# Kernel optimization log

Hardware: AMD Instinct MI355X
Metric: run time of the kernel (lower is better)

## Reference

```python
import jax, jax.numpy as jnp
import numpy as np

D = 1024      # embedding_dim
H = 16        # n_heads
HD = D // H   # head_dim
EPS = 1e-05


def layernorm(x, scale, bias):
    # torch.var default is unbiased (ddof=1) in the original module
    mean = jnp.mean(x, axis=-1, keepdims=True)
    var = jnp.var(x, axis=-1, keepdims=True, ddof=1)
    return scale * (x - mean) / jnp.sqrt(var + EPS) + bias


def gelu(x):
    return 0.5 * x * (1 + jnp.tanh(0.79788456 * (x + 0.044715 * x ** 3)))


def setup_inputs() -> dict:
    key = jax.random.key(0)
    ks = jax.random.split(key, 12)
    s = 0.02
    return {
        "x": jax.random.normal(ks[0], (2, 2048, D), dtype=jnp.float32),
        "Wq": jax.random.normal(ks[1], (D, D), dtype=jnp.float32) * s,
        "Wk": jax.random.normal(ks[2], (D, D), dtype=jnp.float32) * s,
        "Wv": jax.random.normal(ks[3], (D, D), dtype=jnp.float32) * s,
        "Wo": jax.random.normal(ks[4], (D, D), dtype=jnp.float32) * s,
        "bo": jnp.zeros((D,), dtype=jnp.float32),
        "W1": jax.random.normal(ks[5], (D, 4 * D), dtype=jnp.float32) * s,
        "b1": jnp.zeros((4 * D,), dtype=jnp.float32),
        "W2": jax.random.normal(ks[6], (4 * D, D), dtype=jnp.float32) * s,
        "b2": jnp.zeros((D,), dtype=jnp.float32),
        "ln1_scale": jnp.ones((D,), dtype=jnp.float32),
        "ln1_bias": jnp.zeros((D,), dtype=jnp.float32),
        "ln2_scale": jnp.ones((D,), dtype=jnp.float32),
        "ln2_bias": jnp.zeros((D,), dtype=jnp.float32),
    }


def reference(x, Wq, Wk, Wv, Wo, bo, W1, b1, W2, b2,
              ln1_scale, ln1_bias, ln2_scale, ln2_bias):
    B, S, _ = x.shape
    # --- attention sub-block (pre-LN) ---
    h = layernorm(x, ln1_scale, ln1_bias)
    q = (h @ Wq).reshape(B, S, H, HD).transpose(0, 2, 1, 3)  # [B,H,S,HD]
    k = (h @ Wk).reshape(B, S, H, HD).transpose(0, 2, 1, 3)
    v = (h @ Wv).reshape(B, S, H, HD).transpose(0, 2, 1, 3)
    scores = jnp.einsum("bhqd,bhkd->bhqk", q, k)             # [B,H,S,S]
    causal = jnp.tril(jnp.ones((S, S), dtype=bool))
    scores = jnp.where(causal, scores, -jnp.inf)
    attn = jax.nn.softmax(scores / jnp.sqrt(jnp.float32(HD)), axis=-1)
    ctx = jnp.einsum("bhqk,bhkd->bhqd", attn, v)
    ctx = ctx.transpose(0, 2, 1, 3).reshape(B, S, H * HD)
    x = x + (ctx @ Wo + bo)
    # --- FFN sub-block (pre-LN) ---
    h = layernorm(x, ln2_scale, ln2_bias)
    x = x + (gelu(h @ W1 + b1) @ W2 + b2)
    return x
```

## Files before the change

### kernel.cpp

```cpp
#include <hip/hip_runtime.h>
#include <hip/hip_bf16.h>
#include <cstdint>

#define D_DIM 1024
#define S_DIM 2048
#define B_DIM 2
#define NROWS 4096
#define H_DIM 16
#define LOG2E 1.4426950408889634f
#define QSCALE (0.125f * LOG2E)

typedef __bf16 bf16x8 __attribute__((ext_vector_type(8)));
typedef float f32x4 __attribute__((ext_vector_type(4)));
typedef unsigned short u16x8 __attribute__((ext_vector_type(8)));

#define MFMA16(a, b, c) __builtin_amdgcn_mfma_f32_16x16x32_bf16(a, b, c, 0, 0, 0)
#define SBM __builtin_amdgcn_sched_barrier(0x0F)
#define WBAR __builtin_amdgcn_s_barrier()
#define VMW(n) asm volatile("s_waitcnt vmcnt(" #n ")" ::: "memory")

__device__ __forceinline__ void async_cp16(const void* g, void* lds) {
  __builtin_amdgcn_global_load_lds(
      (const __attribute__((address_space(1))) void*)(uintptr_t)g,
      (__attribute__((address_space(3))) void*)(uint32_t)(uintptr_t)lds, 16, 0, 0);
}

__device__ __forceinline__ unsigned short f2bf(float f) {
  __hip_bfloat16 h = __float2bfloat16(f);
  return __builtin_bit_cast(unsigned short, h);
}

__device__ __forceinline__ float bf2f(unsigned short u) {
  return __builtin_bit_cast(float, (unsigned int)u << 16);
}

__device__ __forceinline__ float gelu_fast(float v) {
  float u = v * v;
  float w = v * fmaf(u, 0.044715f, 1.f);
  float e = exp2f(w * -2.3022161f);
  return v * __builtin_amdgcn_rcpf(1.f + e);
}

struct TcArgs {
  const float* src[6];
  __hip_bfloat16* dst[6];
  int K[6];
  int N[6];
  int start[6];
};

__global__ __launch_bounds__(256) void transpose_cast6_kernel(TcArgs a) {
  __shared__ float tile[32][33];
  int bid = blockIdx.x, mi = 0;
#pragma unroll
  for (int i = 1; i < 6; i++)
    if (bid >= a.start[i]) mi = i;
  const float* W = a.src[mi];
  __hip_bfloat16* Wt = a.dst[mi];
  int K = a.K[mi], N = a.N[mi];
  int rel = bid - a.start[mi];
  int tilesx = N >> 5;
  int shift = (N == 4096) ? 7 : 5;
  int n0 = (rel & (tilesx - 1)) * 32, k0 = (rel >> shift) * 32;
  int tx = threadIdx.x, ty = threadIdx.y;
#pragma unroll
  for (int i = 0; i < 32; i += 8)
    tile[ty + i][tx] = W[(size_t)(k0 + ty + i) * N + n0 + tx];
  __syncthreads();
#pragma unroll
  for (int i = 0; i < 32; i += 8)
    Wt[(size_t)(n0 + ty + i) * K + k0 + tx] = __float2bfloat16(tile[tx][ty + i]);
}

__global__ __launch_bounds__(256) void ln_kernel(
    const float* __restrict__ x, const float* __restrict__ sc,
    const float* __restrict__ bi, __hip_bfloat16* __restrict__ out) {
  int row = blockIdx.x, t = threadIdx.x;
  float4 v = ((const float4*)(x + (size_t)row * D_DIM))[t];
  float s = v.x + v.y + v.z + v.w;
  float ss = v.x * v.x + v.y * v.y + v.z * v.z + v.w * v.w;
#pragma unroll
  for (int off = 32; off > 0; off >>= 1) {
    s += __shfl_xor(s, off);
    ss += __shfl_xor(ss, off);
  }
  __shared__ float red[8];
  int wid = t >> 6;
  if ((t & 63) == 0) { red[wid] = s; red[4 + wid] = ss; }
  __syncthreads();
  s = red[0] + red[1] + red[2] + red[3];
  ss = red[4] + red[5] + red[6] + red[7];
  float mean = s * (1.f / 1024.f);
  float var = (ss - 1024.f * mean * mean) * (1.f / 1023.f);
  float inv = rsqrtf(var + 1e-5f);
  float4 scv = ((const float4*)sc)[t];
  float4 biv = ((const float4*)bi)[t];
  ushort4 o;
  o.x = f2bf(scv.x * (v.x - mean) * inv + biv.x);
  o.y = f2bf(scv.y * (v.y - mean) * inv + biv.y);
  o.z = f2bf(scv.z * (v.z - mean) * inv + biv.z);
  o.w = f2bf(scv.w * (v.w - mean) * inv + biv.w);
  ((ushort4*)(out + (size_t)row * D_DIM))[t] = o;
}

template <int EPI>
__global__ __launch_bounds__(512) void gemm256_kernel(
    const __hip_bfloat16* __restrict__ A, const __hip_bfloat16* __restrict__ Bt,
    void* __restrict__ Cout, const float* __restrict__ bias,
    __hip_bfloat16* __restrict__ qb, __hip_bfloat16* __restrict__ kb,
    unsigned short* __restrict__ vt, int strideA, int strideB) {
  __shared__ char lds[131072];
  const int t = threadIdx.x;
  const int lane = t & 63, wid = t >> 6;
  const int ql = lane & 15, g = lane >> 4;
  const int wr = wid >> 2, wc = wid & 3;
  const int m0 = blockIdx.x * 256, n0 = blockIdx.y * 256;
  const int koff = blockIdx.z * 1024;
  const int sw = (ql & 7) << 4;

  const int srow = t >> 3;
  const int scol = ((t & 7) << 4) ^ ((srow & 7) << 4);
  const __hip_bfloat16* aBase = A + (size_t)(m0 + srow) * strideA + koff + (scol >> 1);
  const __hip_bfloat16* bBase = Bt + (size_t)(n0 + srow) * strideB + koff + (scol >> 1);
  const uint32_t ldsT = (uint32_t)(t * 16);

  auto stgA = [&](int kt, int h) {
    char* dst = lds + (((kt & 1) * 2 + h) * 16384) + ldsT;
    const __hip_bfloat16* src = aBase + (size_t)(h * 128) * strideA + kt * 64;
    async_cp16(src, dst);
    async_cp16(src + (size_t)64 * strideA, dst + 8192);
  };
  auto stgB = [&](int kt, int h) {
    char* dst = lds + 65536 + (((kt & 1) * 2 + h) * 16384) + ldsT;
    const __hip_bfloat16* src = bBase + (size_t)(h * 128) * strideB + kt * 64;
    async_cp16(src, dst);
    async_cp16(src + (size_t)64 * strideB, dst + 8192);
  };

  bf16x8 aR[4][2], bR[2][2][2];
  f32x4 acc[2][4][2][2] = {};

  auto ldA = [&](int slot, int mh) {
    const char* base = lds + ((slot * 2 + mh) * 16384) + (wr * 64 + ql) * 128;
#pragma unroll
    for (int mi = 0; mi < 4; mi++)
#pragma unroll
      for (int kk = 0; kk < 2; kk++)
        aR[mi][kk] = *(const bf16x8*)(base + mi * 2048 + ((kk * 64 + g * 16) ^ sw));
  };
  auto ldB = [&](int slot, int nh) {
    const char* base = lds + 65536 + ((slot * 2 + nh) * 16384) + (wc * 32 + ql) * 128;
#pragma unroll
    for (int ni = 0; ni < 2; ni++)
#pragma unroll
      for (int kk = 0; kk < 2; kk++)
        bR[nh][ni][kk] = *(const bf16x8*)(base + ni * 2048 + ((kk * 64 + g * 16) ^ sw));
  };
  auto mma = [&](int mh, int nh) {
    __builtin_amdgcn_s_setprio(1);
#pragma unroll
    for (int mi = 0; mi < 4; mi++)
#pragma unroll
      for (int ni = 0; ni < 2; ni++) {
        f32x4 c = acc[mh][mi][nh][ni];
        c = MFMA16(aR[mi][0], bR[nh][ni][0], c);
        c = MFMA16(aR[mi][1], bR[nh][ni][1], c);
        acc[mh][mi][nh][ni] = c;
      }
    __builtin_amdgcn_s_setprio(0);
  };

  stgB(0, 0); stgA(0, 0); stgB(0, 1); stgA(0, 1); stgB(1, 0);
  VMW(6); SBM; WBAR;

#pragma unroll 1
  for (int i = 0; i < 7; i++) {
    const int o = 2 * i + 1, e2 = 2 * i + 2, o2 = 2 * i + 3;
    ldA(0, 0); ldB(0, 0); stgA(o, 0);  VMW(6); SBM; WBAR; mma(0, 0);
    ldB(0, 1);            stgB(o, 1);  VMW(6); SBM; WBAR; mma(0, 1);
    ldA(0, 1);            stgA(o, 1);          SBM; WBAR; mma(1, 1);
                          stgB(e2, 0); VMW(6); SBM; WBAR; mma(1, 0);
    ldA(1, 0); ldB(1, 0); stgA(e2, 0); VMW(6); SBM; WBAR; mma(0, 0);
    ldB(1, 1);            stgB(e2, 1); VMW(6); SBM; WBAR; mma(0, 1);
    ldA(1, 1);            stgA(e2, 1);         SBM; WBAR; mma(1, 1);
                          stgB(o2, 0); VMW(6); SBM; WBAR; mma(1, 0);
  }
  ldA(0, 0); ldB(0, 0); stgA(15, 0); VMW(6); SBM; WBAR; mma(0, 0);
  ldB(0, 1);            stgB(15, 1); VMW(6); SBM; WBAR; mma(0, 1);
  ldA(0, 1);            stgA(15, 1);         SBM; WBAR; mma(1, 1);
                                     VMW(4); SBM; WBAR; mma(1, 0);
  ldA(1, 0); ldB(1, 0);              VMW(2); SBM; WBAR; mma(0, 0);
  ldB(1, 1);                         VMW(0); SBM; WBAR; mma(0, 1);
  ldA(1, 1);                                 SBM; WBAR; mma(1, 1);
                                                        mma(1, 0);

#pragma unroll
  for (int mh = 0; mh < 2; mh++) {
#pragma unroll
    for (int mi = 0; mi < 4; mi++) {
      const int row0 = m0 + mh * 128 + wr * 64 + mi * 16 + g * 4;
#pragma unroll
      for (int nh = 0; nh < 2; nh++) {
#pragma unroll
        for (int ni = 0; ni < 2; ni++) {
          const int colt = nh * 128 + wc * 32 + ni * 16 + ql;
          const f32x4 c = acc[mh][mi][nh][ni];
          if (EPI == 0) {
            const int seg = n0 >> 10;
            const int c1k = (n0 & 1023) + colt;
            if (seg < 2) {
              __hip_bfloat16* Ob = seg == 0 ? qb : kb;
              const float sc = seg == 0 ? QSCALE : 1.f;
#pragma unroll
              for (int rr = 0; rr < 4; rr++)
                Ob[(size_t)(row0 + rr) * 1024 + c1k] = __float2bfloat16(c[rr] * sc);
            } else {
              const int h = c1k >> 6, dh = c1k & 63;
              const int bb = row0 >> 11, s0 = row0 & 2047;
              ushort4 pk;
              pk.x = f2bf(c[0]); pk.y = f2bf(c[1]); pk.z = f2bf(c[2]); pk.w = f2bf(c[3]);
              *(ushort4*)(vt + (((size_t)(bb * 16 + h) * 64 + dh) << 11) + s0) = pk;
            }
          } else if (EPI == 1) {
            const int col = n0 + colt;
            const float bv = bias[col];
#pragma unroll
            for (int rr = 0; rr < 4; rr++)
              ((__hip_bfloat16*)Cout)[(size_t)(row0 + rr) * 4096 + col] =
                  __float2bfloat16(gelu_fast(c[rr] + bv));
          } else {
            unsigned short* Cp = (unsigned short*)Cout + (size_t)blockIdx.z * NROWS * 1024;
            const int col = n0 + colt;
#pragma unroll
            for (int rr = 0; rr < 4; rr++)
              Cp[(size_t)(row0 + rr) * 1024 + col] = f2bf(c[rr]);
          }
        }
      }
    }
  }
}

template <int BN, int EPI>
__global__ __launch_bounds__(256) void gemm_bt_kernel(
    const __hip_bfloat16* __restrict__ A, const __hip_bfloat16* __restrict__ Bt,
    void* __restrict__ Cout, const float* __restrict__ bias,
    const float* __restrict__ resid, int M, int N, int K, int kchunk) {
  constexpr int NBF = BN / 32;
  __shared__ __hip_bfloat16 As[2][128 * 32];
  __shared__ __hip_bfloat16 Bs[2][BN * 32];
  const int t = threadIdx.x;
  const int lane = t & 63, wid = t >> 6;
  const int ql = lane & 15, g = lane >> 4;
  const int m0 = blockIdx.x * 128, n0 = blockIdx.y * BN;
  const int kz = blockIdx.z;
  const int wm = (wid >> 1) * 64, wn = (wid & 1) * (BN / 2);
  f32x4 acc[4][NBF] = {};
  const int sr = t >> 2, sc8 = (t & 3) * 8;
  const __hip_bfloat16* ag = A + (size_t)(m0 + sr) * K + sc8 + (size_t)kz * kchunk;
  const __hip_bfloat16* bg = Bt + (size_t)(n0 + sr) * K + sc8 + (size_t)kz * kchunk;

  auto stage = [&](int buf, int k0) {
    async_cp16(ag + k0, (char*)&As[buf][0] + wid * 1024);
    async_cp16(ag + (size_t)64 * K + k0, (char*)&As[buf][0] + 4096 + wid * 1024);
    async_cp16(bg + k0, (char*)&Bs[buf][0] + wid * 1024);
    if constexpr (BN == 128)
      async_cp16(bg + (size_t)64 * K + k0, (char*)&Bs[buf][0] + 4096 + wid * 1024);
  };
  auto compute = [&](int buf) {
    bf16x8 af[4], bfr[NBF];
#pragma unroll
    for (int mb = 0; mb < 4; mb++)
      af[mb] = *(const bf16x8*)(&As[buf][(wm + mb * 16 + ql) * 32 + g * 8]);
#pragma unroll
    for (int nb = 0; nb < NBF; nb++)
      bfr[nb] = *(const bf16x8*)(&Bs[buf][(wn + nb * 16 + ql) * 32 + g * 8]);
#pragma unroll
    for (int mb = 0; mb < 4; mb++)
#pragma unroll
      for (int nb = 0; nb < NBF; nb++)
        acc[mb][nb] = MFMA16(af[mb], bfr[nb], acc[mb][nb]);
  };

  stage(0, 0);
  __syncthreads();
  const int nsteps = kchunk >> 5;
  int cur = 0;
  for (int s = 0; s < nsteps - 1; ++s) {
    stage(cur ^ 1, (s + 1) * 32);
    compute(cur);
    __syncthreads();
    cur ^= 1;
  }
  compute(cur);

  const int rb = m0 + wm + (g << 2);
  const int cb = n0 + wn + ql;
#pragma unroll
  for (int mb = 0; mb < 4; mb++) {
#pragma unroll
    for (int nb = 0; nb < NBF; nb++) {
      int col = cb + nb * 16;
#pragma unroll
      for (int r = 0; r < 4; r++) {
        int row = rb + mb * 16 + r;
        float v = acc[mb][nb][r];
        if (EPI == 1) {
          ((float*)Cout)[(size_t)row * N + col] =
              v + bias[col] + resid[(size_t)row * N + col];
        }
      }
    }
  }
}

__global__ __launch_bounds__(256) void ffn2_reduce_kernel(
    const unsigned short* __restrict__ parts, const float* __restrict__ bias,
    const float* __restrict__ resid, float* __restrict__ out) {
  const size_t i = ((size_t)blockIdx.x * 256 + threadIdx.x) * 8;
  const int col = (int)(i & 1023);
  float a[8];
  float4 r0 = *(const float4*)(resid + i);
  float4 r1 = *(const float4*)(resid + i + 4);
  float4 b0 = *(const float4*)(bias + col);
  float4 b1 = *(const float4*)(bias + col + 4);
  a[0] = r0.x + b0.x; a[1] = r0.y + b0.y; a[2] = r0.z + b0.z; a[3] = r0.w + b0.w;
  a[4] = r1.x + b1.x; a[5] = r1.y + b1.y; a[6] = r1.z + b1.z; a[7] = r1.w + b1.w;
#pragma unroll
  for (int c = 0; c < 4; c++) {
    u16x8 p = *(const u16x8*)(parts + (size_t)c * ((size_t)NROWS * 1024) + i);
#pragma unroll
    for (int j = 0; j < 8; j++) a[j] += bf2f(p[j]);
  }
  float4 o0 = {a[0], a[1], a[2], a[3]};
  float4 o1 = {a[4], a[5], a[6], a[7]};
  *(float4*)(out + i) = o0;
  *(float4*)(out + i + 4) = o1;
}

__global__ __launch_bounds__(256) void attn_kernel(
    const __hip_bfloat16* __restrict__ Q, const __hip_bfloat16* __restrict__ Kb,
    const __hip_bfloat16* __restrict__ Vt, __hip_bfloat16* __restrict__ ctx) {
  __shared__ unsigned short Ks[2][64 * 64];
  __shared__ unsigned short Vs[2][64 * 64];
  __shared__ alignas(16) unsigned short Ps[4][16 * 64];
  const int t = threadIdx.x;
  const int lane = t & 63, wid = t >> 6;
  const int ql = lane & 15, g = lane >> 4;
  const int bid = blockIdx.x;
  const int r4 = bid >> 8, k8 = (bid >> 5) & 7, bh = bid & 31;
  const int qt = (r4 == 0) ? 31 - k8 : (r4 == 1) ? 16 + k8 : (r4 == 2) ? 15 - k8 : k8;
  const int b = bh >> 4, hh = bh & 15;
  const int wq0 = qt * 64 + wid * 16;
  const __hip_bfloat16* qp = Q + (size_t)b * S_DIM * D_DIM + hh * 64;
  const __hip_bfloat16* kp = Kb + (size_t)b * S_DIM * D_DIM + hh * 64;
  const __hip_bfloat16* vp = Vt + (size_t)bh * 64 * S_DIM;
  const int kvend = qt * 64 + 64;
  const int swz = (ql & 7) << 4;
  const f32x4 z4 = {0.f, 0.f, 0.f, 0.f};

  auto stageKV = [&](int buf, int kv0) {
    const int sub = lane >> 3, c = lane & 7;
#pragma unroll
    for (int i = 0; i < 2; i++) {
      const int row = wid * 16 + i * 8 + sub;
      const int cs = (c ^ (row & 7)) * 8;
      async_cp16(kp + (size_t)(kv0 + row) * D_DIM + cs,
                 (char*)&Ks[buf][0] + (wid * 16 + i * 8) * 128);
      async_cp16(vp + (size_t)row * S_DIM + kv0 + cs,
                 (char*)&Vs[buf][0] + (wid * 16 + i * 8) * 128);
    }
  };

  bf16x8 qf[2];
#pragma unroll
  for (int hf = 0; hf < 2; hf++)
    qf[hf] = *(const bf16x8*)(qp + (size_t)(wq0 + ql) * D_DIM + hf * 32 + g * 8);

  float m = -3.0e38f, lsum = 0.f;
  f32x4 acc[4] = {};
  unsigned short* Pw = Ps[wid];

  stageKV(0, 0);
  __syncthreads();
  int cur = 0;
  for (int kv0 = 0; kv0 < kvend; kv0 += 64) {
    if (kv0 + 64 < kvend) stageKV(cur ^ 1, kv0 + 64);

    if (kv0 <= wq0 + 15) {
      const char* Kt = (const char*)&Ks[cur][0];
      f32x4 st[4];
#pragma unroll
      for (int ks = 0; ks < 4; ks++) {
        bf16x8 k0 = *(const bf16x8*)(Kt + (ks * 16 + ql) * 128 + ((g * 16) ^ swz));
        bf16x8 k1 = *(const bf16x8*)(Kt + (ks * 16 + ql) * 128 + (((4 + g) * 16) ^ swz));
        st[ks] = MFMA16(k1, qf[1], MFMA16(k0, qf[0], z4));
      }
      if (kv0 + 63 > wq0) {
#pragma unroll
        for (int ks = 0; ks < 4; ks++)
#pragma unroll
          for (int r = 0; r < 4; r++)
            if (kv0 + ks * 16 + 4 * g + r > wq0 + ql) st[ks][r] = -3.0e38f;
      }
      float tm = -3.0e38f;
#pragma unroll
      for (int ks = 0; ks < 4; ks++)
#pragma unroll
        for (int r = 0; r < 4; r++) tm = fmaxf(tm, st[ks][r]);
      tm = fmaxf(tm, __shfl_xor(tm, 16));
      tm = fmaxf(tm, __shfl_xor(tm, 32));
      if (!__all(tm <= m + 8.f)) {
        const float mn = fmaxf(m, tm);
        const float alpha = exp2f(m - mn);
        lsum *= alpha;
#pragma unroll
        for (int db = 0; db < 4; db++) acc[db] *= alpha;
        m = mn;
      }
      float psum = 0.f;
#pragma unroll
      for (int ks = 0; ks < 4; ks++) {
        float p0 = exp2f(st[ks][0] - m), p1 = exp2f(st[ks][1] - m);
        float p2 = exp2f(st[ks][2] - m), p3 = exp2f(st[ks][3] - m);
        psum += (p0 + p1) + (p2 + p3);
        ushort4 pk;
        pk.x = f2bf(p0); pk.y = f2bf(p1); pk.z = f2bf(p2); pk.w = f2bf(p3);
        *(ushort4*)((char*)Pw + ql * 128 + ((ks * 32 + 8 * g) ^ swz)) = pk;
      }
      psum += __shfl_xor(psum, 16);
      psum += __shfl_xor(psum, 32);
      lsum += psum;

      const char* Vtl = (const char*)&Vs[cur][0];
#pragma unroll
      for (int ksl = 0; ksl < 2; ksl++) {
        bf16x8 pb = *(const bf16x8*)((const char*)Pw + ql * 128 + ((ksl * 64 + 16 * g) ^ swz));
#pragma unroll
        for (int db = 0; db < 4; db++) {
          bf16x8 va = *(const bf16x8*)(Vtl + (db * 16 + ql) * 128 + (((ksl * 4 + g) * 16) ^ swz));
          acc[db] = MFMA16(va, pb, acc[db]);
        }
      }
    }
    __syncthreads();
    cur ^= 1;
  }

  const float inv = 1.f / lsum;
  unsigned short* cp = (unsigned short*)ctx + (size_t)(b * S_DIM + wq0 + ql) * D_DIM + hh * 64;
#pragma unroll
  for (int db = 0; db < 4; db++)
#pragma unroll
    for (int i = 0; i < 2; i++) {
      unsigned int lo = f2bf(acc[db][2 * i] * inv);
      unsigned int hi = f2bf(acc[db][2 * i + 1] * inv);
      *(unsigned int*)(cp + db * 16 + 4 * g + 2 * i) = lo | (hi << 16);
    }
}

extern "C" void kernel_launch(void* const* d_in, const int* in_sizes, int n_in,
                              void* d_out, int out_size, void* d_ws, size_t ws_size,
                              hipStream_t stream) {
  const float* x = (const float*)d_in[0];
  const float* Wq = (const float*)d_in[1];
  const float* Wk = (const float*)d_in[2];
  const float* Wv = (const float*)d_in[3];
  const float* Wo = (const float*)d_in[4];
  const float* bo = (const float*)d_in[5];
  const float* W1 = (const float*)d_in[6];
  const float* b1 = (const float*)d_in[7];
  const float* W2 = (const float*)d_in[8];
  const float* b2 = (const float*)d_in[9];
  const float* ln1s = (const float*)d_in[10];
  const float* ln1b = (const float*)d_in[11];
  const float* ln2s = (const float*)d_in[12];
  const float* ln2b = (const float*)d_in[13];
  float* out = (float*)d_out;

  char* p = (char*)d_ws;
  auto take = [&](size_t n) { char* r = p; p += (n + 255) & ~(size_t)255; return r; };
  __hip_bfloat16* Wqt = (__hip_bfloat16*)take((size_t)1024 * 1024 * 2);
  __hip_bfloat16* Wkt = (__hip_bfloat16*)take((size_t)1024 * 1024 * 2);
  __hip_bfloat16* Wvt = (__hip_bfloat16*)take((size_t)1024 * 1024 * 2);
  __hip_bfloat16* Wot = (__hip_bfloat16*)take((size_t)1024 * 1024 * 2);
  __hip_bfloat16* W1t = (__hip_bfloat16*)take((size_t)4096 * 1024 * 2);
  __hip_bfloat16* W2t = (__hip_bfloat16*)take((size_t)4096 * 1024 * 2);
  __hip_bfloat16* hbuf = (__hip_bfloat16*)take((size_t)NROWS * 1024 * 2);
  __hip_bfloat16* qbuf = (__hip_bfloat16*)take((size_t)NROWS * 1024 * 2);
  __hip_bfloat16* kbuf = (__hip_bfloat16*)take((size_t)NROWS * 1024 * 2);
  __hip_bfloat16* vtbuf = (__hip_bfloat16*)take((size_t)NROWS * 1024 * 2);
  __hip_bfloat16* ctxbuf = (__hip_bfloat16*)take((size_t)NROWS * 1024 * 2);
  float* x1buf = (float*)take((size_t)NROWS * 1024 * 4);
  __hip_bfloat16* h2buf = (__hip_bfloat16*)take((size_t)NROWS * 1024 * 2);
  __hip_bfloat16* gbuf = (__hip_bfloat16*)take((size_t)NROWS * 4096 * 2);
  unsigned short* parts = (unsigned short*)hbuf;

  TcArgs ta;
  ta.src[0] = Wq;  ta.dst[0] = Wqt;  ta.K[0] = 1024; ta.N[0] = 1024; ta.start[0] = 0;
  ta.src[1] = Wk;  ta.dst[1] = Wkt;  ta.K[1] = 1024; ta.N[1] = 1024; ta.start[1] = 1024;
  ta.src[2] = Wv;  ta.dst[2] = Wvt;  ta.K[2] = 1024; ta.N[2] = 1024; ta.start[2] = 2048;
  ta.src[3] = Wo;  ta.dst[3] = Wot;  ta.K[3] = 1024; ta.N[3] = 1024; ta.start[3] = 3072;
  ta.src[4] = W1;  ta.dst[4] = W1t;  ta.K[4] = 1024; ta.N[4] = 4096; ta.start[4] = 4096;
  ta.src[5] = W2;  ta.dst[5] = W2t;  ta.K[5] = 4096; ta.N[5] = 1024; ta.start[5] = 8192;
  transpose_cast6_kernel<<<12288, dim3(32, 8), 0, stream>>>(ta);

  ln_kernel<<<NROWS, 256, 0, stream>>>(x, ln1s, ln1b, hbuf);

  gemm256_kernel<0><<<dim3(16, 12), 512, 0, stream>>>(
      hbuf, Wqt, nullptr, nullptr, qbuf, kbuf, (unsigned short*)vtbuf, 1024, 1024);

  attn_kernel<<<1024, 256, 0, stream>>>(qbuf, kbuf, vtbuf, ctxbuf);

  gemm_bt_kernel<64, 1><<<dim3(32, 16, 1), 256, 0, stream>>>(
      ctxbuf, Wot, x1buf, bo, x, NROWS, 1024, 1024, 1024);

  ln_kernel<<<NROWS, 256, 0, stream>>>(x1buf, ln2s, ln2b, h2buf);

  gemm256_kernel<1><<<dim3(16, 16), 512, 0, stream>>>(
      h2buf, W1t, gbuf, b1, nullptr, nullptr, nullptr, 1024, 1024);

  gemm256_kernel<2><<<dim3(16, 4, 4), 512, 0, stream>>>(
      gbuf, W2t, parts, nullptr, nullptr, nullptr, nullptr, 4096, 4096);

  ffn2_reduce_kernel<<<2048, 256, 0, stream>>>(parts, b2, x1buf, out);
}
```

Baseline: 209.7 us.

## Restructure GEMM main loop staging order with deeper prefetch and extra barriers

Reorders the global-to-LDS staging so more stages are in flight (vmcnt waits raised from 6 to 10, prologue prefetches seven chunks) and changes which A/B halves are loaded at each step. Each MFMA phase now waits for LDS reads explicitly and adds a trailing workgroup barrier, replacing the scheduling barriers. The aim is more latency hiding for global loads. In exchange it doubles the barrier count per phase and serializes LDS reads before the math, which may add stalls.

```diff
diff --git a/kernel.cpp b/kernel.cpp
--- a/kernel.cpp
+++ b/kernel.cpp
@@ -15,8 +15,8 @@
 typedef unsigned short u16x8 __attribute__((ext_vector_type(8)));
 
 #define MFMA16(a, b, c) __builtin_amdgcn_mfma_f32_16x16x32_bf16(a, b, c, 0, 0, 0)
-#define SBM __builtin_amdgcn_sched_barrier(0x0F)
 #define WBAR __builtin_amdgcn_s_barrier()
+#define LGKM0 { asm volatile("s_waitcnt lgkmcnt(0)" ::: "memory"); __builtin_amdgcn_sched_barrier(0); }
 #define VMW(n) asm volatile("s_waitcnt vmcnt(" #n ")" ::: "memory")
 
 __device__ __forceinline__ void async_cp16(const void* g, void* lds) {
@@ -170,29 +170,30 @@
     __builtin_amdgcn_s_setprio(0);
   };
 
-  stgB(0, 0); stgA(0, 0); stgB(0, 1); stgA(0, 1); stgB(1, 0);
-  VMW(6); SBM; WBAR;
+  stgA(0, 0); stgB(0, 0); stgB(0, 1); stgA(0, 1);
+  stgA(1, 0); stgB(1, 0); stgB(1, 1);
+  VMW(10); WBAR;
 
 #pragma unroll 1
   for (int i = 0; i < 7; i++) {
-    const int o = 2 * i + 1, e2 = 2 * i + 2, o2 = 2 * i + 3;
-    ldA(0, 0); ldB(0, 0); stgA(o, 0);  VMW(6); SBM; WBAR; mma(0, 0);
-    ldB(0, 1);            stgB(o, 1);  VMW(6); SBM; WBAR; mma(0, 1);
-    ldA(0, 1);            stgA(o, 1);          SBM; WBAR; mma(1, 1);
-                          stgB(e2, 0); VMW(6); SBM; WBAR; mma(1, 0);
-    ldA(1, 0); ldB(1, 0); stgA(e2, 0); VMW(6); SBM; WBAR; mma(0, 0);
-    ldB(1, 1);            stgB(e2, 1); VMW(6); SBM; WBAR; mma(0, 1);
-    ldA(1, 1);            stgA(e2, 1);         SBM; WBAR; mma(1, 1);
-                          stgB(o2, 0); VMW(6); SBM; WBAR; mma(1, 0);
-  }
-  ldA(0, 0); ldB(0, 0); stgA(15, 0); VMW(6); SBM; WBAR; mma(0, 0);
-  ldB(0, 1);            stgB(15, 1); VMW(6); SBM; WBAR; mma(0, 1);
-  ldA(0, 1);            stgA(15, 1);         SBM; WBAR; mma(1, 1);
-                                     VMW(4); SBM; WBAR; mma(1, 0);
-  ldA(1, 0); ldB(1, 0);              VMW(2); SBM; WBAR; mma(0, 0);
-  ldB(1, 1);                         VMW(0); SBM; WBAR; mma(0, 1);
-  ldA(1, 1);                                 SBM; WBAR; mma(1, 1);
-                                                        mma(1, 0);
+    const int e = 2 * i, o = 2 * i + 1;
+    ldA(0, 0); ldB(0, 0); stgA(o, 1);     VMW(10); WBAR; LGKM0; mma(0, 0); WBAR;
+    ldB(0, 1);            stgA(e + 2, 0); VMW(10); WBAR; LGKM0; mma(0, 1); WBAR;
+    ldA(0, 1);            stgB(e + 2, 0);          WBAR; LGKM0; mma(1, 1); WBAR;
+                          stgB(e + 2, 1); VMW(10); WBAR;        mma(1, 0); WBAR;
+    ldA(1, 0); ldB(1, 0); stgA(o + 1, 1); VMW(10); WBAR; LGKM0; mma(0, 0); WBAR;
+    ldB(1, 1);            stgA(o + 2, 0); VMW(10); WBAR; LGKM0; mma(0, 1); WBAR;
+    ldA(1, 1);            stgB(o + 2, 0);          WBAR; LGKM0; mma(1, 1); WBAR;
+                          stgB(o + 2, 1); VMW(10); WBAR;        mma(1, 0); WBAR;
+  }
+  ldA(0, 0); ldB(0, 0); stgA(15, 1); VMW(10); WBAR; LGKM0; mma(0, 0); WBAR;
+  ldB(0, 1);                         VMW(8);  WBAR; LGKM0; mma(0, 1); WBAR;
+  ldA(0, 1);                                  WBAR; LGKM0; mma(1, 1); WBAR;
+                                     VMW(4);  WBAR;        mma(1, 0); WBAR;
+  ldA(1, 0); ldB(1, 0);              VMW(2);  WBAR; LGKM0; mma(0, 0); WBAR;
+  ldB(1, 1);                         VMW(0);  WBAR; LGKM0; mma(0, 1); WBAR;
+  ldA(1, 1);                                  WBAR; LGKM0; mma(1, 1); WBAR;
+                                                           mma(1, 0);
 
 #pragma unroll
   for (int mh = 0; mh < 2; mh++) {
```

After: 204.5 us. 2.5% less time.

## Restructure GEMM main loop to whole-tile prefetch and swizzle block order

Applied to the files above, without the earlier changes.

Replaces the fine-grained half-tile staging schedule in the 256x256 GEMM with a simpler per-k-tile loop. Each iteration reads the full current slot into registers, waits on LDS, then issues all four async copies for tile kt+2 while running the second half of the MFMAs. This cuts the number of barriers per k-tile. It also remaps the block index with a stride-by-eighths permutation to change which tiles run concurrently, presumably for XCD/L2 locality. The trade-off is coarser overlap, since only two barriers per tile give less interleaving of loads and math, and the old sched_barrier masks become full sched barriers.

```diff
diff --git a/kernel.cpp b/kernel.cpp
--- a/kernel.cpp
+++ b/kernel.cpp
@@ -15,8 +15,9 @@
 typedef unsigned short u16x8 __attribute__((ext_vector_type(8)));
 
 #define MFMA16(a, b, c) __builtin_amdgcn_mfma_f32_16x16x32_bf16(a, b, c, 0, 0, 0)
-#define SBM __builtin_amdgcn_sched_barrier(0x0F)
 #define WBAR __builtin_amdgcn_s_barrier()
+#define SB0 __builtin_amdgcn_sched_barrier(0)
+#define LGKM0 { asm volatile("s_waitcnt lgkmcnt(0)" ::: "memory"); SB0; }
 #define VMW(n) asm volatile("s_waitcnt vmcnt(" #n ")" ::: "memory")
 
 __device__ __forceinline__ void async_cp16(const void* g, void* lds) {
@@ -114,7 +115,11 @@
   const int lane = t & 63, wid = t >> 6;
   const int ql = lane & 15, g = lane >> 4;
   const int wr = wid >> 2, wc = wid & 3;
-  const int m0 = blockIdx.x * 256, n0 = blockIdx.y * 256;
+  const int nbx = gridDim.x;
+  const int lin = blockIdx.y * nbx + blockIdx.x;
+  const int q8 = (nbx * gridDim.y) >> 3;
+  const int sz = (lin & 7) * q8 + (lin >> 3);
+  const int m0 = (sz % nbx) * 256, n0 = (sz / nbx) * 256;
   const int koff = blockIdx.z * 1024;
   const int sw = (ql & 7) << 4;
 
@@ -136,6 +141,7 @@
     async_cp16(src, dst);
     async_cp16(src + (size_t)64 * strideB, dst + 8192);
   };
+  auto stg4 = [&](int kt) { stgA(kt, 0); stgA(kt, 1); stgB(kt, 0); stgB(kt, 1); };
 
   bf16x8 aR[4][2], bR[2][2][2];
   f32x4 acc[2][4][2][2] = {};
@@ -170,29 +176,30 @@
     __builtin_amdgcn_s_setprio(0);
   };
 
-  stgB(0, 0); stgA(0, 0); stgB(0, 1); stgA(0, 1); stgB(1, 0);
-  VMW(6); SBM; WBAR;
+  stg4(0); stg4(1);
+  VMW(8); WBAR;
 
 #pragma unroll 1
-  for (int i = 0; i < 7; i++) {
-    const int o = 2 * i + 1, e2 = 2 * i + 2, o2 = 2 * i + 3;
-    ldA(0, 0); ldB(0, 0); stgA(o, 0);  VMW(6); SBM; WBAR; mma(0, 0);
-    ldB(0, 1);            stgB(o, 1);  VMW(6); SBM; WBAR; mma(0, 1);
-    ldA(0, 1);            stgA(o, 1);          SBM; WBAR; mma(1, 1);
-                          stgB(e2, 0); VMW(6); SBM; WBAR; mma(1, 0);
-    ldA(1, 0); ldB(1, 0); stgA(e2, 0); VMW(6); SBM; WBAR; mma(0, 0);
-    ldB(1, 1);            stgB(e2, 1); VMW(6); SBM; WBAR; mma(0, 1);
-    ldA(1, 1);            stgA(e2, 1);         SBM; WBAR; mma(1, 1);
-                          stgB(o2, 0); VMW(6); SBM; WBAR; mma(1, 0);
-  }
-  ldA(0, 0); ldB(0, 0); stgA(15, 0); VMW(6); SBM; WBAR; mma(0, 0);
-  ldB(0, 1);            stgB(15, 1); VMW(6); SBM; WBAR; mma(0, 1);
-  ldA(0, 1);            stgA(15, 1);         SBM; WBAR; mma(1, 1);
-                                     VMW(4); SBM; WBAR; mma(1, 0);
-  ldA(1, 0); ldB(1, 0);              VMW(2); SBM; WBAR; mma(0, 0);
-  ldB(1, 1);                         VMW(0); SBM; WBAR; mma(0, 1);
-  ldA(1, 1);                                 SBM; WBAR; mma(1, 1);
-                                                        mma(1, 0);
+  for (int kt = 0; kt < 14; ++kt) {
+    const int s = kt & 1;
+    ldA(s, 0); ldB(s, 0); ldB(s, 1);
+    LGKM0; mma(0, 0); mma(0, 1);
+    ldA(s, 1);
+    LGKM0; WBAR; SB0;
+    stg4(kt + 2);
+    mma(1, 1); mma(1, 0);
+    VMW(8); WBAR;
+  }
+  ldA(0, 0); ldB(0, 0); ldB(0, 1);
+  LGKM0; mma(0, 0); mma(0, 1);
+  ldA(0, 1);
+  LGKM0; WBAR;
+  mma(1, 1); mma(1, 0);
+  VMW(0); WBAR;
+  ldA(1, 0); ldB(1, 0); ldB(1, 1);
+  LGKM0; mma(0, 0); mma(0, 1);
+  ldA(1, 1);
+  LGKM0; mma(1, 1); mma(1, 0);
 
 #pragma unroll
   for (int mh = 0; mh < 2; mh++) {
```

Result: no change. 207.2 us (-1.2%).
